# Performance work log

Hardware: AMD Instinct MI355X
Metric: run time of the kernel (lower is better)

Reference implementation:

```python
import jax, jax.numpy as jnp
import numpy as np

B, S, F, H, A = 256, 128, 512, 1024, 18


def setup_inputs() -> dict:
    key = jax.random.key(0)
    ks = jax.random.split(key, 16)
    u = lambda k, shape, fan: jax.random.uniform(k, shape, jnp.float32, -1.0, 1.0) / np.sqrt(fan)
    return {
        "obs": jax.random.normal(ks[0], (B, S, F), jnp.float32),
        "hx": jax.random.normal(ks[1], (B, H), jnp.float32),
        "cx": jax.random.normal(ks[2], (B, H), jnp.float32),
        "behaviour_acts": jax.random.randint(ks[3], (B, S, 1), 0, A),
        "W1": u(ks[4], (H, F), F), "b1": u(ks[5], (H,), F),
        "W_ih": u(ks[6], (4 * H, H), H), "b_ih": u(ks[7], (4 * H,), H),
        "W_hh": u(ks[8], (4 * H, H), H), "b_hh": u(ks[9], (4 * H,), H),
        "W_v": u(ks[10], (1, H), H), "b_v": u(ks[11], (1,), H),
        "W_l": u(ks[12], (A, H), H), "b_l": u(ks[13], (A,), H),
    }


def reference(obs, hx, cx, behaviour_acts, W1, b1, W_ih, b_ih, W_hh, b_hh, W_v, b_v, W_l, b_l):
    # MLP body: [B,S,F] -> [B,S,H]
    x = jax.nn.relu(jnp.einsum("bsf,hf->bsh", obs, W1) + b1)
    # precompute input-to-gate projection for all timesteps (one big GEMM)
    xg = jnp.einsum("bsh,gh->bsg", x, W_ih) + b_ih  # [B,S,4H]

    def step(carry, xg_t):
        h, c = carry
        gates = xg_t + h @ W_hh.T + b_hh  # [B,4H], gate order i,f,g,o (torch LSTMCell)
        i, f, g, o = jnp.split(gates, 4, axis=-1)
        c = jax.nn.sigmoid(f) * c + jax.nn.sigmoid(i) * jnp.tanh(g)
        h = jax.nn.sigmoid(o) * jnp.tanh(c)
        return (h, c), h

    _, hs = jax.lax.scan(step, (hx, cx), jnp.swapaxes(xg, 0, 1))
    output = jnp.swapaxes(hs, 0, 1)  # [B,S,H]

    value = output @ W_v.T + b_v  # [B,S,1]
    logits = output @ W_l.T + b_l  # [B,S,A]
    # torch Categorical(probs=softmax(logits)) => log-prob via log_softmax
    logp = jax.nn.log_softmax(logits, axis=-1)
    acts = behaviour_acts.reshape(logits.shape[0], logits.shape[1], 1)
    log_probs = jnp.take_along_axis(logp, acts, axis=-1)  # [B,S,1]
    entropy = -jnp.sum(jnp.exp(logp) * logp, axis=-1, keepdims=True)  # [B,S,1]
    return log_probs, entropy, value
```

## Files before the change

kernel.cpp:

```cpp
#include <hip/hip_runtime.h>

#define B_ 256
#define S_ 128
#define SP1 (S_+1)
#define F_ 512
#define H_ 1024
#define A_ 18
#define M_ (B_*S_)
#define G_ (4*H_)
#define CH_ 16
#define CR_ (B_*CH_)

typedef unsigned short u16;
typedef __attribute__((ext_vector_type(8))) _Float16 f16x8;
typedef __attribute__((ext_vector_type(4))) _Float16 f16x4;
typedef __attribute__((ext_vector_type(8))) short   s16x8;
typedef __attribute__((ext_vector_type(4))) float f32x4;
typedef __attribute__((ext_vector_type(4))) unsigned int u32x4;

__device__ __forceinline__ float bf2f(u16 u){
  union{unsigned int i; float f;} v; v.i=((unsigned int)u)<<16; return v.f;
}
__device__ __forceinline__ u16 f2bf(float f){
  unsigned int i=__float_as_uint(f);
  unsigned int r=(i+0x7fffu+((i>>16)&1u))>>16;
  return (u16)r;
}
__device__ __forceinline__ u16 f2h(float f){
  _Float16 h=(_Float16)f;
  union{_Float16 h; u16 u;} v; v.h=h; return v.u;
}
__device__ __forceinline__ float ldf(const void* p, size_t i, int m){
  return m ? ((const float*)p)[i] : bf2f(((const u16*)p)[i]);
}
__device__ __forceinline__ f16x8 load8_h(const void* base, size_t off, int m){
  f16x8 v;
  if(m==2) return *(const f16x8*)((const u16*)base + off);
  if(m==1){
    const float* f=(const float*)base + off;
    float4 a=*(const float4*)f; float4 b=*(const float4*)(f+4);
    v[0]=(_Float16)a.x; v[1]=(_Float16)a.y; v[2]=(_Float16)a.z; v[3]=(_Float16)a.w;
    v[4]=(_Float16)b.x; v[5]=(_Float16)b.y; v[6]=(_Float16)b.z; v[7]=(_Float16)b.w;
    return v;
  }
  s16x8 w=*(const s16x8*)((const u16*)base + off);
#pragma unroll
  for(int k=0;k<8;k++) v[k]=(_Float16)bf2f((u16)w[k]);
  return v;
}

__device__ __forceinline__ void store_c2(u16* p, u16 v){
  unsigned int vv=v;
  asm volatile("global_store_short %0, %1, off sc0 sc1" :: "v"(p), "v"(vv) : "memory");
}
__device__ __forceinline__ int load_c4(const int* p){
  int r;
  asm volatile("global_load_dword %0, %1, off sc0 sc1" : "=v"(r) : "v"(p));
  return r;
}
__device__ __forceinline__ void store_c4(int* p, int v){
  asm volatile("global_store_dword %0, %1, off sc0 sc1" :: "v"(p), "v"(v) : "memory");
}

__device__ __forceinline__ void bar_flags32(int* flags, int target, int gi, int lane, int w){
  asm volatile("s_waitcnt vmcnt(0)" ::: "memory");
  __syncthreads();
  if(w==0){
    if(lane==0) store_c4(flags+gi, target);
    while(true){
      int v=load_c4(flags+(lane&31));
      asm volatile("s_waitcnt vmcnt(0)" ::: "memory");
      if(__all(v>=target)) break;
      __builtin_amdgcn_s_sleep(1);
    }
  }
  __syncthreads();
}

template<int ROWS, int MAP>
__device__ __forceinline__ void stage(const void* base, int mode, int lda, int k0,
                                      int rowoff, int t0, u16* lds, int tid){
  if(mode==2){
    constexpr int NI=(ROWS*8)/256;
    int wv=tid>>6, l=tid&63;
#pragma unroll
    for(int i=0;i<NI;i++){
      int s0=i*256+(wv<<6), s=s0+l;
      int r=s>>3, gc=(s&7)^(r&7);
      int p=rowoff+r, sr;
      if(MAP==0)      sr=p;
      else if(MAP==1) sr=(p&3)*H_+(p>>2);
      else            sr=(p>>4)*S_+t0+(p&15);
      const u16* src=(const u16*)base + (size_t)sr*lda + k0 + gc*8;
      u16* dst=lds + s0*8;
      __builtin_amdgcn_global_load_lds((const __attribute__((address_space(1))) unsigned int*)src,
                                       (__attribute__((address_space(3))) unsigned int*)dst,
                                       16, 0, 0);
    }
  } else {
#pragma unroll
    for(int s0=tid; s0<ROWS*8; s0+=256){
      int r=s0>>3, gc=s0&7, lc=gc^(r&7);
      int p=rowoff+r, sr;
      if(MAP==0)      sr=p;
      else if(MAP==1) sr=(p&3)*H_+(p>>2);
      else            sr=(p>>4)*S_+t0+(p&15);
      f16x8 v=load8_h(base, (size_t)sr*lda + k0 + gc*8, mode);
      *(f16x8*)(lds + r*64 + lc*8)=v;
    }
  }
}

__device__ __forceinline__ f16x8 frag_ld(const u16* lds, int r0, int kc, int lane){
  int r = r0 + (lane&15);
  int c = (kc + (lane>>4)) ^ (r&7);
  return *(const f16x8*)(lds + r*64 + c*8);
}

template<int AMAP, int BMAP, int OUTMODE>
__global__ __launch_bounds__(256,3) void gemm128(const void* A, const void* Bt, void* C,
    const float* __restrict__ biasf, const int* __restrict__ flag,
    int K, int lda, int ldb, int ldc, int t0, int amode, int bmode){
  int m=*flag;
  int am = amode<0 ? m : amode;
  int bm_ = bmode<0 ? m : bmode;
  __shared__ u16 As[128*64];
  __shared__ u16 Bs[128*64];
  int tid=threadIdx.x, lane=tid&63, w=tid>>6;
  int bm=blockIdx.y*128, bn=blockIdx.x*128;
  int wm=(w&1)*64, wn=(w>>1)*64;
  f32x4 acc[4][4];
#pragma unroll
  for(int i=0;i<4;i++)
#pragma unroll
    for(int j=0;j<4;j++) acc[i][j]=(f32x4)(0.f);
  for(int k0=0;k0<K;k0+=64){
    stage<128,AMAP>(A , am,  lda, k0, bm, t0, As, tid);
    stage<128,BMAP>(Bt, bm_, ldb, k0, bn, t0, Bs, tid);
    __syncthreads();
#pragma unroll
    for(int kk=0;kk<2;kk++){
      f16x8 af[4], bq[4];
#pragma unroll
      for(int i=0;i<4;i++) af[i]=frag_ld(As, wm+i*16, kk*4, lane);
#pragma unroll
      for(int j=0;j<4;j++) bq[j]=frag_ld(Bs, wn+j*16, kk*4, lane);
#pragma unroll
      for(int i=0;i<4;i++)
#pragma unroll
        for(int j=0;j<4;j++)
          acc[i][j]=__builtin_amdgcn_mfma_f32_16x16x32_f16(af[i],bq[j],acc[i][j],0,0,0);
    }
    __syncthreads();
  }
  int rl=lane>>4, cl=lane&15;
#pragma unroll
  for(int j=0;j<4;j++){
    int col=bn+wn+j*16+cl;
    float bb=biasf[col];
#pragma unroll
    for(int i=0;i<4;i++){
#pragma unroll
      for(int r=0;r<4;r++){
        int row=bm+wm+i*16+rl*4+r;
        float v=acc[i][j][r]+bb;
        if(OUTMODE==0){ v=fmaxf(v,0.f); ((u16*)C)[(size_t)row*ldc+col]=f2h(v); }
        else if(OUTMODE==2){ ((u16*)C)[(size_t)row*ldc+col]=f2h(v); }
        else { ((float*)C)[(size_t)row*ldc+col]=v; }
      }
    }
  }
}

__global__ __launch_bounds__(512,2) void lstm_persist(u16* __restrict__ hh,
        const u16* __restrict__ Whhp, const u16* __restrict__ xgp,
        float* __restrict__ cst, int* __restrict__ cntc, int tbase){
  __shared__ u16 As[16*2048];
  __shared__ float gs[32*132];
  int tid=threadIdx.x, lane=tid&63, w=tid>>6;
  int grp=blockIdx.x&7, ci=blockIdx.x>>3;
  int bm=grp*32, bn=ci*128;
  int* flags = cntc + grp*64;

  f16x8 bw[32];
#pragma unroll
  for(int t=0;t<32;t++){
    int p = bn + w*16 + (lane&15);
    int k = t*32 + (lane>>4)*8;
    bw[t]=*(const f16x8*)(Whhp + (size_t)p*H_ + k);
  }
#pragma unroll
  for(int t=0;t<32;t++) asm volatile("" : "+a"(bw[t]));

  int rl0=tid>>5, rl1=(tid+512)>>5, u0=tid&31;
  int gu=(bn>>2)+u0;
  float c0=cst[(size_t)(bm+rl0)*H_+gu];
  float c1=cst[(size_t)(bm+rl1)*H_+gu];

  for(int dt=0;dt<CH_;dt++){
    f16x4 xv0=*(const f16x4*)(xgp + ((size_t)(bm+rl0)*CH_+dt)*G_ + bn + u0*4);
    f16x4 xv1=*(const f16x4*)(xgp + ((size_t)(bm+rl1)*CH_+dt)*G_ + bn + u0*4);
    if(dt) bar_flags32(flags, tbase+dt, ci, lane, w);
    const u16* hbase = hh + (size_t)(tbase+dt)*H_;
    {
      u32x4 tmp[4];
#pragma unroll
      for(int i=0;i<4;i++){
        int s=tid+i*512, kt=s>>8, r=(s>>3)&31, gc=s&7;
        tmp[i]=*(const u32x4*)(hbase + (size_t)(bm+r)*(SP1*H_) + kt*64 + gc*8);
      }
#pragma unroll
      for(int i=0;i<4;i++){
        int s=tid+i*512, kt=s>>8, r=(s>>3)&31, gc=s&7, lc=gc^(r&7);
        *(u32x4*)(As + kt*2048 + r*64 + lc*8)=tmp[i];
      }
    }
    __syncthreads();
    u32x4 tmp2[4];
#pragma unroll
    for(int i=0;i<4;i++){
      int s=tid+(i+4)*512, kt=s>>8, r=(s>>3)&31, gc=s&7;
      tmp2[i]=*(const u32x4*)(hbase + (size_t)(bm+r)*(SP1*H_) + kt*64 + gc*8);
    }
    f32x4 acc0=(f32x4)(0.f), acc1=(f32x4)(0.f);
#pragma unroll
    for(int t=0;t<16;t++){
      int kt=t>>1, kk=t&1;
      f16x8 af0=frag_ld(As+kt*2048, 0,  kk*4, lane);
      f16x8 af1=frag_ld(As+kt*2048, 16, kk*4, lane);
      acc0=__builtin_amdgcn_mfma_f32_16x16x32_f16(af0,bw[t],acc0,0,0,0);
      acc1=__builtin_amdgcn_mfma_f32_16x16x32_f16(af1,bw[t],acc1,0,0,0);
    }
#pragma unroll
    for(int i=0;i<4;i++){
      int s=tid+(i+4)*512, kt=s>>8, r=(s>>3)&31, gc=s&7, lc=gc^(r&7);
      *(u32x4*)(As + kt*2048 + r*64 + lc*8)=tmp2[i];
    }
    __syncthreads();
#pragma unroll
    for(int t=16;t<32;t++){
      int kt=t>>1, kk=t&1;
      f16x8 af0=frag_ld(As+kt*2048, 0,  kk*4, lane);
      f16x8 af1=frag_ld(As+kt*2048, 16, kk*4, lane);
      acc0=__builtin_amdgcn_mfma_f32_16x16x32_f16(af0,bw[t],acc0,0,0,0);
      acc1=__builtin_amdgcn_mfma_f32_16x16x32_f16(af1,bw[t],acc1,0,0,0);
    }
#pragma unroll
    for(int r=0;r<4;r++){
      gs[(   (lane>>4)*4+r)*132 + w*16+(lane&15)]=acc0[r];
      gs[(16+(lane>>4)*4+r)*132 + w*16+(lane&15)]=acc1[r];
    }
    __syncthreads();
    {
      float4 gv=*(const float4*)&gs[rl0*132+u0*4];
      float ii=1.f/(1.f+__expf(-(gv.x+(float)xv0[0])));
      float ff=1.f/(1.f+__expf(-(gv.y+(float)xv0[1])));
      float gg=1.f-2.f/(__expf(2.f*(gv.z+(float)xv0[2]))+1.f);
      float oo=1.f/(1.f+__expf(-(gv.w+(float)xv0[3])));
      c0=ff*c0+ii*gg;
      float th=1.f-2.f/(__expf(2.f*c0)+1.f);
      store_c2(hh + ((size_t)(bm+rl0)*SP1 + tbase+dt+1)*H_ + gu, f2h(oo*th));
    }
    {
      float4 gv=*(const float4*)&gs[rl1*132+u0*4];
      float ii=1.f/(1.f+__expf(-(gv.x+(float)xv1[0])));
      float ff=1.f/(1.f+__expf(-(gv.y+(float)xv1[1])));
      float gg=1.f-2.f/(__expf(2.f*(gv.z+(float)xv1[2]))+1.f);
      float oo=1.f/(1.f+__expf(-(gv.w+(float)xv1[3])));
      c1=ff*c1+ii*gg;
      float th=1.f-2.f/(__expf(2.f*c1)+1.f);
      store_c2(hh + ((size_t)(bm+rl1)*SP1 + tbase+dt+1)*H_ + gu, f2h(oo*th));
    }
  }
  cst[(size_t)(bm+rl0)*H_+gu]=c0;
  cst[(size_t)(bm+rl1)*H_+gu]=c1;
}

__global__ __launch_bounds__(256,2) void lstm_step(u16* __restrict__ hh, int slotAbs, int dt,
        const void* __restrict__ Whh, const u16* __restrict__ xg,
        float* __restrict__ cst, const int* __restrict__ flag){
  int m=*flag;
  __shared__ u16 As[64*64];
  __shared__ u16 Bs[64*64];
  __shared__ float gs[64*64];
  int tid=threadIdx.x, lane=tid&63, w=tid>>6;
  int bm=blockIdx.y*64, bn=blockIdx.x*64;
  int wm=(w&1)*32, wn=(w>>1)*32;
  f32x4 acc[2][2];
#pragma unroll
  for(int i=0;i<2;i++)
#pragma unroll
    for(int j=0;j<2;j++) acc[i][j]=(f32x4)(0.f);
  for(int k0=0;k0<H_;k0+=64){
    stage<64,0>(hh + (size_t)slotAbs*H_, 2, SP1*H_, k0, bm, 0, As, tid);
    stage<64,1>(Whh,                     m, H_,     k0, bn, 0, Bs, tid);
    __syncthreads();
#pragma unroll
    for(int kk=0;kk<2;kk++){
      f16x8 af[2], bq[2];
#pragma unroll
      for(int i=0;i<2;i++) af[i]=frag_ld(As, wm+i*16, kk*4, lane);
#pragma unroll
      for(int j=0;j<2;j++) bq[j]=frag_ld(Bs, wn+j*16, kk*4, lane);
#pragma unroll
      for(int i=0;i<2;i++)
#pragma unroll
        for(int j=0;j<2;j++)
          acc[i][j]=__builtin_amdgcn_mfma_f32_16x16x32_f16(af[i],bq[j],acc[i][j],0,0,0);
    }
    __syncthreads();
  }
  int rl=lane>>4, cl=lane&15;
#pragma unroll
  for(int j=0;j<2;j++){
    int coll=wn+j*16+cl;
#pragma unroll
    for(int i=0;i<2;i++){
#pragma unroll
      for(int r=0;r<4;r++){
        int rowl=wm+i*16+rl*4+r;
        float xv=(float)((const _Float16*)xg)[((size_t)(bm+rowl)*CH_+dt)*G_ + bn+coll];
        gs[rowl*64+coll]=acc[i][j][r] + xv;
      }
    }
  }
  __syncthreads();
#pragma unroll
  for(int p=0;p<4;p++){
    int idx=p*256+tid;
    int rowl=idx>>4, u=idx&15;
    float4 gv = *(const float4*)&gs[rowl*64+u*4];
    float ii=1.f/(1.f+__expf(-gv.x));
    float ff=1.f/(1.f+__expf(-gv.y));
    float gg=1.f-2.f/(__expf(2.f*gv.z)+1.f);
    float oo=1.f/(1.f+__expf(-gv.w));
    int gb=bm+rowl;
    int gu=(bn>>2)+u;
    size_t ci=(size_t)gb*H_+gu;
    float cn=ff*cst[ci]+ii*gg;
    cst[ci]=cn;
    float th=1.f-2.f/(__expf(2.f*cn)+1.f);
    hh[((size_t)gb*SP1 + slotAbs+1)*H_ + gu]=f2h(oo*th);
  }
}

__global__ __launch_bounds__(512,1) void heads_gemm(const u16* __restrict__ hh,
      const u16* __restrict__ WH, const float* __restrict__ blf,
      const int* __restrict__ acts, void* __restrict__ out, const int* __restrict__ flag){
  int m=*flag;
  __shared__ u16 Bs[16*2048];
  __shared__ u16 As[128*64];
  __shared__ float gs[128*36];
  int tid=threadIdx.x, lane=tid&63, w=tid>>6;
  int bm=blockIdx.x*128;
#pragma unroll
  for(int i=0;i<8;i++){
    int s=tid+i*512;
    int kt=s>>8, r=(s>>3)&31, gc=s&7, lc=gc^(r&7);
    *(f16x8*)(Bs+kt*2048+r*64+lc*8) = *(const f16x8*)(WH + (size_t)r*H_ + kt*64 + gc*8);
  }
  f32x4 acc0=(f32x4)(0.f), acc1=(f32x4)(0.f);
  for(int kt=0;kt<16;kt++){
#pragma unroll
    for(int i=0;i<2;i++){
      int s0=i*512+(w<<6), s=s0+lane;
      int r=s>>3, gc=(s&7)^(r&7);
      int rg=bm+r;
      const u16* src=hh + ((size_t)(rg>>7)*SP1 + (rg&127)+1)*H_ + kt*64 + gc*8;
      u16* dst=As + s0*8;
      __builtin_amdgcn_global_load_lds((const __attribute__((address_space(1))) unsigned int*)src,
                                       (__attribute__((address_space(3))) unsigned int*)dst,
                                       16, 0, 0);
    }
    __syncthreads();
#pragma unroll
    for(int kk=0;kk<2;kk++){
      f16x8 af=frag_ld(As, w*16, kk*4, lane);
      f16x8 b0=frag_ld(Bs+kt*2048, 0,  kk*4, lane);
      f16x8 b1=frag_ld(Bs+kt*2048, 16, kk*4, lane);
      acc0=__builtin_amdgcn_mfma_f32_16x16x32_f16(af,b0,acc0,0,0,0);
      acc1=__builtin_amdgcn_mfma_f32_16x16x32_f16(af,b1,acc1,0,0,0);
    }
    __syncthreads();
  }
#pragma unroll
  for(int r=0;r<4;r++){
    gs[(w*16+(lane>>4)*4+r)*36 + (lane&15)]      = acc0[r];
    gs[(w*16+(lane>>4)*4+r)*36 + 16 + (lane&15)] = acc1[r];
  }
  __syncthreads();
  if(tid<128){
    int rg=bm+tid;
    float lg[18];
#pragma unroll
    for(int j=0;j<18;j++) lg[j]=gs[tid*36+j]+blf[j];
    float value=gs[tid*36+18]+blf[18];
    float mx=lg[0];
#pragma unroll
    for(int j=1;j<18;j++) mx=fmaxf(mx,lg[j]);
    float se=0.f, s1=0.f;
#pragma unroll
    for(int j=0;j<18;j++){ float e=__expf(lg[j]-mx); se+=e; s1+=e*(lg[j]-mx); }
    float lse=__logf(se);
    int a=acts[rg];
    float la=0.f;
#pragma unroll
    for(int j=0;j<18;j++) la = (j==a) ? lg[j] : la;
    float lp=la-mx-lse;
    float ent=lse - s1/se;
    if(m){
      ((float*)out)[rg]=lp; ((float*)out)[M_+rg]=ent; ((float*)out)[2*M_+rg]=value;
    } else {
      ((u16*)out)[rg]=f2bf(lp); ((u16*)out)[M_+rg]=f2bf(ent); ((u16*)out)[2*M_+rg]=f2bf(value);
    }
  }
}

__global__ __launch_bounds__(256,2) void heads_full(const u16* __restrict__ hh,
      const void* __restrict__ Wl, const void* __restrict__ Wv,
      const float* __restrict__ blf, const int* __restrict__ acts,
      void* __restrict__ out, const int* __restrict__ flag){
  int m=*flag;
  int rg = blockIdx.x*4 + (threadIdx.x>>6);
  int lane = threadIdx.x & 63;
  int b=rg>>7, t=rg&(S_-1);
  const u16* h = hh + ((size_t)b*SP1 + t+1)*H_;
  f16x8 h0=*(const f16x8*)(h + lane*16), h1=*(const f16x8*)(h + lane*16 + 8);
  float hv[16];
#pragma unroll
  for(int k=0;k<8;k++){ hv[k]=(float)h0[k]; hv[8+k]=(float)h1[k]; }
  float dots[19];
#pragma unroll
  for(int j=0;j<19;j++){
    const void* wrow = (j<18) ? Wl : Wv;
    size_t roff = (j<18) ? (size_t)j*H_ : 0;
    float wv_[16];
    if(m){
      const float* f=(const float*)wrow + roff + lane*16;
      float4 a=*(const float4*)f, b2=*(const float4*)(f+4), c=*(const float4*)(f+8), d=*(const float4*)(f+12);
      wv_[0]=a.x;wv_[1]=a.y;wv_[2]=a.z;wv_[3]=a.w; wv_[4]=b2.x;wv_[5]=b2.y;wv_[6]=b2.z;wv_[7]=b2.w;
      wv_[8]=c.x;wv_[9]=c.y;wv_[10]=c.z;wv_[11]=c.w; wv_[12]=d.x;wv_[13]=d.y;wv_[14]=d.z;wv_[15]=d.w;
    } else {
      const u16* ub=(const u16*)wrow + roff + lane*16;
      s16x8 w0=*(const s16x8*)ub, w1=*(const s16x8*)(ub+8);
#pragma unroll
      for(int k=0;k<8;k++){ wv_[k]=bf2f((u16)w0[k]); wv_[8+k]=bf2f((u16)w1[k]); }
    }
    float d=0.f;
#pragma unroll
    for(int k=0;k<16;k++) d += hv[k]*wv_[k];
#pragma unroll
    for(int mm=1;mm<64;mm<<=1) d += __shfl_xor(d, mm, 64);
    dots[j]=d;
  }
  float lg[18];
#pragma unroll
  for(int j=0;j<18;j++) lg[j]=dots[j]+blf[j];
  float value=dots[18]+blf[18];
  float mx=lg[0];
#pragma unroll
  for(int j=1;j<18;j++) mx=fmaxf(mx,lg[j]);
  float se=0.f, s1=0.f;
#pragma unroll
  for(int j=0;j<18;j++){ float e=__expf(lg[j]-mx); se+=e; s1+=e*(lg[j]-mx); }
  float lse=__logf(se);
  int a=acts[rg];
  float la=0.f;
#pragma unroll
  for(int j=0;j<18;j++) la = (j==a) ? lg[j] : la;
  float lp=la-mx-lse;
  float ent=lse - s1/se;
  if(lane==0){
    if(m){
      ((float*)out)[rg]=lp; ((float*)out)[M_+rg]=ent; ((float*)out)[2*M_+rg]=value;
    } else {
      ((u16*)out)[rg]=f2bf(lp); ((u16*)out)[M_+rg]=f2bf(ent); ((u16*)out)[2*M_+rg]=f2bf(value);
    }
  }
}

__global__ void detect(const u16* __restrict__ obs_w, int* __restrict__ flag){
  __shared__ float red[256];
  float mx=0.f;
  for(int i=threadIdx.x;i<4096;i+=256) mx=fmaxf(mx,fabsf(bf2f(obs_w[i])));
  red[threadIdx.x]=mx; __syncthreads();
  for(int s=128;s>0;s>>=1){
    if(threadIdx.x<s) red[threadIdx.x]=fmaxf(red[threadIdx.x],red[threadIdx.x+s]);
    __syncthreads();
  }
  if(threadIdx.x==0) *flag=(red[0]>1e4f)?1:0;
}

__global__ void prep(const void* bih, const void* bhh, const void* b1, const void* bl, const void* bv,
                     const void* cx, const void* hx,
                     float* biasg, float* b1f, float* blf, float* cst, u16* hh,
                     int* cnt, const int* __restrict__ flag){
  int m=*flag;
  size_t i=(size_t)blockIdx.x*256+threadIdx.x;
  if(i<G_){ size_t rm=(i&3)*H_+(i>>2); biasg[i]=ldf(bih,rm,m)+ldf(bhh,rm,m); return; }
  i-=G_;
  if(i<H_){ b1f[i]=ldf(b1,i,m); return; }
  i-=H_;
  if(i<19){ blf[i]=(i<18)?ldf(bl,i,m):ldf(bv,0,m); return; }
  i-=19;
  if(i<512){ cnt[i]=0; return; }
  i-=512;
  if(i<(size_t)B_*H_){ cst[i]=ldf(cx,i,m); return; }
  i-=(size_t)B_*H_;
  if(i<(size_t)B_*H_){
    size_t b=i>>10, k=i&1023;
    hh[b*(SP1*H_) + k]=f2h(ldf(hx,i,m));
  }
}

__global__ void convw(const void* W1, const void* Wih, const void* Whh,
                      const void* Wl, const void* Wv,
                      u16* W1h, u16* Wihp, u16* Whhp, u16* WH,
                      const int* __restrict__ flag){
  int m=*flag;
  size_t i=((size_t)blockIdx.x*256+threadIdx.x)*8;
  const size_t n1=(size_t)H_*F_, n2=(size_t)G_*H_, n3=(size_t)32*H_;
  if(i<n1){ *(f16x8*)(W1h+i)=load8_h(W1,i,m); return; }
  i-=n1;
  if(i<n2){ size_t p=i>>10, c=i&1023; size_t sr=(p&3)*H_+(p>>2);
            *(f16x8*)(Wihp+i)=load8_h(Wih, sr*H_+c, m); return; }
  i-=n2;
  if(i<n2){ size_t p=i>>10, c=i&1023; size_t sr=(p&3)*H_+(p>>2);
            *(f16x8*)(Whhp+i)=load8_h(Whh, sr*H_+c, m); return; }
  i-=n2;
  if(i<n3){
    size_t j=i>>10, c=i&1023;
    f16x8 v;
    if(j<18)      v=load8_h(Wl, j*H_+c, m);
    else if(j==18) v=load8_h(Wv, c, m);
    else{ for(int k=0;k<8;k++) v[k]=(_Float16)0.f; }
    *(f16x8*)(WH+i)=v;
  }
}
__global__ void convobs(const void* obs, u16* obsh, const int* __restrict__ flag){
  int m=*flag;
  size_t i=((size_t)blockIdx.x*256+threadIdx.x)*8;
  if(i<(size_t)M_*F_) *(f16x8*)(obsh+i)=load8_h(obs,i,m);
}

extern "C" void kernel_launch(void* const* d_in, const int* in_sizes, int n_in,
                              void* d_out, int out_size, void* d_ws, size_t ws_size,
                              hipStream_t stream){
  const void* obs=d_in[0];
  const void* hx =d_in[1];
  const void* cx =d_in[2];
  const int* acts=(const int*)d_in[3];
  const void* W1 =d_in[4];
  const void* b1 =d_in[5];
  const void* Wih=d_in[6];
  const void* bih=d_in[7];
  const void* Whh=d_in[8];
  const void* bhh=d_in[9];
  const void* Wv =d_in[10];
  const void* bv =d_in[11];
  const void* Wl =d_in[12];
  const void* bl =d_in[13];

  char* w=(char*)d_ws;
  auto alloc=[&](size_t n){ char* p=w; w+=((n+255)&~(size_t)255); return p; };
  int*   flag =(int*)alloc(4);
  int*   cnt  =(int*)alloc(512*4);
  float* biasg=(float*)alloc((size_t)G_*4);
  float* b1f  =(float*)alloc((size_t)H_*4);
  float* blf  =(float*)alloc(32*4);
  float* cst  =(float*)alloc((size_t)B_*H_*4);
  u16*   hh   =(u16*)alloc((size_t)B_*SP1*H_*2);
  u16*   xc   =(u16*)alloc((size_t)CR_*H_*2);
  u16*   xg   =(u16*)alloc((size_t)CR_*G_*2);
  size_t nW=((size_t)H_*F_ + 2*(size_t)G_*H_ + 32*(size_t)H_)*2 + 1024;
  bool pathW = ((size_t)(w-(char*)d_ws) + nW) <= ws_size;
  u16 *W1h=0,*Wihp=0,*Whhp=0,*WH=0;
  if(pathW){ W1h=(u16*)alloc((size_t)H_*F_*2); Wihp=(u16*)alloc((size_t)G_*H_*2);
             Whhp=(u16*)alloc((size_t)G_*H_*2); WH=(u16*)alloc((size_t)32*H_*2); }
  size_t nXC=(size_t)M_*H_*2 + 256;
  bool pathXC = pathW && (((size_t)(w-(char*)d_ws) + nXC) <= ws_size);
  u16* xcf=0; if(pathXC) xcf=(u16*)alloc((size_t)M_*H_*2);
  size_t nO=(size_t)M_*F_*2 + 256;
  bool pathO = pathXC && (((size_t)(w-(char*)d_ws) + nO) <= ws_size);
  u16* obsh=0; if(pathO) obsh=(u16*)alloc((size_t)M_*F_*2);

  detect<<<1,256,0,stream>>>((const u16*)obs, flag);
  {
    int total=G_+H_+19+512+B_*H_+B_*H_;
    prep<<<(total+255)/256,256,0,stream>>>(bih,bhh,b1,bl,bv,cx,hx, biasg,b1f,blf,cst,hh,cnt, flag);
  }
  if(pathW){
    size_t n=((size_t)H_*F_+2*(size_t)G_*H_+32*(size_t)H_)/8;
    convw<<<(int)((n+255)/256),256,0,stream>>>(W1,Wih,Whh,Wl,Wv, W1h,Wihp,Whhp,WH, flag);
  }
  if(pathO){
    size_t n=(size_t)M_*F_/8;
    convobs<<<(int)((n+255)/256),256,0,stream>>>(obs, obsh, flag);
  }
  if(pathXC){
    gemm128<0,0,0><<<dim3(H_/128, M_/128),256,0,stream>>>(
        pathO?(const void*)obsh:obs, pathW?(const void*)W1h:W1, xcf, b1f, flag,
        F_, F_, F_, H_, 0, pathO?2:-1, pathW?2:-1);
  }

  const int NC=S_/CH_;
  for(int c=0;c<NC;c++){
    int t0=c*CH_;
    if(!pathXC){
      gemm128<2,0,0><<<dim3(H_/128, CR_/128),256,0,stream>>>(
          obs, pathW?(const void*)W1h:W1, xc, b1f, flag, F_, F_, F_, H_, t0, -1, pathW?2:-1);
    }
    if(pathXC)
      gemm128<2,0,2><<<dim3(G_/128, CR_/128),256,0,stream>>>(
          xcf, Wihp, xg, biasg, flag, H_, H_, H_, G_, t0, 2, 2);
    else if(pathW)
      gemm128<0,0,2><<<dim3(G_/128, CR_/128),256,0,stream>>>(
          xc, Wihp, xg, biasg, flag, H_, H_, H_, G_, 0, 2, 2);
    else
      gemm128<0,1,2><<<dim3(G_/128, CR_/128),256,0,stream>>>(
          xc, Wih, xg, biasg, flag, H_, H_, H_, G_, 0, 2, -1);

    if(pathW)
      lstm_persist<<<256,512,0,stream>>>(hh, Whhp, xg, cst, cnt, t0);
    else
      for(int dt=0;dt<CH_;dt++)
        lstm_step<<<dim3(G_/64, B_/64),256,0,stream>>>(hh, t0+dt, dt, Whh, xg, cst, flag);
  }

  if(pathW)
    heads_gemm<<<dim3(M_/128),512,0,stream>>>(hh, WH, blf, acts, d_out, flag);
  else
    heads_full<<<dim3(M_/4),256,0,stream>>>(hh, Wl, Wv, blf, acts, d_out, flag);
}
```

Before: 1.107 ms.

## Overlap next chunk's input-gate GEMM with the persistent LSTM kernel

The persistent LSTM kernel now launches 512 extra blocks beyond its 256 recurrence blocks. These extra blocks compute the next chunk's x·W_ih projection into a double-buffered xg array, so the standalone GEMM launch per chunk is removed after the first chunk. The recurrence LDS buffer is enlarged and shared with the gate scratch, and the h tile is loaded in one pass instead of two halves. Risks include the co-scheduled GEMM blocks competing with the flag-synchronized recurrence blocks for CUs and bandwidth, or preventing those blocks from all becoming resident.

New measurement: 1.162 ms. 1.05x slower.

```diff
diff --git a/kernel.cpp b/kernel.cpp
--- a/kernel.cpp
+++ b/kernel.cpp
@@ -172,12 +172,81 @@
   }
 }
 
-__global__ __launch_bounds__(512,2) void lstm_persist(u16* __restrict__ hh,
+__global__ __launch_bounds__(512,2) void lstm_xg(u16* __restrict__ hh,
         const u16* __restrict__ Whhp, const u16* __restrict__ xgp,
-        float* __restrict__ cst, int* __restrict__ cntc, int tbase){
-  __shared__ u16 As[16*2048];
-  __shared__ float gs[32*132];
+        float* __restrict__ cst, int* __restrict__ cntc, int tbase,
+        const u16* __restrict__ xcf, const u16* __restrict__ Wihp,
+        const float* __restrict__ biasg, u16* __restrict__ xgn, int t0n){
+  __shared__ __align__(16) char lds_raw[16*2048*2];
   int tid=threadIdx.x, lane=tid&63, w=tid>>6;
+
+  if(blockIdx.x>=256){
+    u16* As2=(u16*)lds_raw;
+    u16* Bs2=(u16*)(lds_raw+16384);
+    int gb=blockIdx.x-256;
+    int tm=gb&31, tn=gb>>5;
+    int bm2=tm*128, bn2=tn*256;
+    int wr=w&1, wc=w>>1;
+    f32x4 acc[4][4];
+#pragma unroll
+    for(int i=0;i<4;i++)
+#pragma unroll
+      for(int j=0;j<4;j++) acc[i][j]=(f32x4)(0.f);
+    for(int kt=0;kt<16;kt++){
+      int k0=kt*64;
+#pragma unroll
+      for(int i=0;i<2;i++){
+        int s0=w*128+i*64, s=s0+lane;
+        int r=s>>3, gc=(s&7)^(r&7);
+        int p=bm2+r;
+        const u16* src=xcf + ((size_t)(p>>4)*S_ + t0n + (p&15))*H_ + k0 + gc*8;
+        __builtin_amdgcn_global_load_lds((const __attribute__((address_space(1))) unsigned int*)src,
+                                         (__attribute__((address_space(3))) unsigned int*)(As2+s0*8),
+                                         16, 0, 0);
+      }
+#pragma unroll
+      for(int i=0;i<4;i++){
+        int s0=w*256+i*64, s=s0+lane;
+        int r=s>>3, gc=(s&7)^(r&7);
+        const u16* src=Wihp + (size_t)(bn2+r)*H_ + k0 + gc*8;
+        __builtin_amdgcn_global_load_lds((const __attribute__((address_space(1))) unsigned int*)src,
+                                         (__attribute__((address_space(3))) unsigned int*)(Bs2+s0*8),
+                                         16, 0, 0);
+      }
+      __syncthreads();
+#pragma unroll
+      for(int kk=0;kk<2;kk++){
+        f16x8 af[4], bq[4];
+#pragma unroll
+        for(int i=0;i<4;i++) af[i]=frag_ld(As2, wr*64+i*16, kk*4, lane);
+#pragma unroll
+        for(int j=0;j<4;j++) bq[j]=frag_ld(Bs2, wc*64+j*16, kk*4, lane);
+#pragma unroll
+        for(int i=0;i<4;i++)
+#pragma unroll
+          for(int j=0;j<4;j++)
+            acc[i][j]=__builtin_amdgcn_mfma_f32_16x16x32_f16(af[i],bq[j],acc[i][j],0,0,0);
+      }
+      __syncthreads();
+    }
+    int rl=lane>>4, cl=lane&15;
+#pragma unroll
+    for(int j=0;j<4;j++){
+      int col=bn2+wc*64+j*16+cl;
+      float bb=biasg[col];
+#pragma unroll
+      for(int i=0;i<4;i++){
+#pragma unroll
+        for(int r=0;r<4;r++){
+          int row=bm2+wr*64+i*16+rl*4+r;
+          ((u16*)xgn)[(size_t)row*G_+col]=f2h(acc[i][j][r]+bb);
+        }
+      }
+    }
+    return;
+  }
+  u16* As=(u16*)lds_raw;
+  float* gs=(float*)lds_raw;
   int grp=blockIdx.x&7, ci=blockIdx.x>>3;
   int bm=grp*32, bn=ci*128;
   int* flags = cntc + grp*64;
@@ -203,48 +272,29 @@
     if(dt) bar_flags32(flags, tbase+dt, ci, lane, w);
     const u16* hbase = hh + (size_t)(tbase+dt)*H_;
     {
-      u32x4 tmp[4];
-#pragma unroll
-      for(int i=0;i<4;i++){
+      u32x4 tmp[8];
+#pragma unroll
+      for(int i=0;i<8;i++){
         int s=tid+i*512, kt=s>>8, r=(s>>3)&31, gc=s&7;
         tmp[i]=*(const u32x4*)(hbase + (size_t)(bm+r)*(SP1*H_) + kt*64 + gc*8);
       }
 #pragma unroll
-      for(int i=0;i<4;i++){
+      for(int i=0;i<8;i++){
         int s=tid+i*512, kt=s>>8, r=(s>>3)&31, gc=s&7, lc=gc^(r&7);
         *(u32x4*)(As + kt*2048 + r*64 + lc*8)=tmp[i];
       }
     }
     __syncthreads();
-    u32x4 tmp2[4];
-#pragma unroll
-    for(int i=0;i<4;i++){
-      int s=tid+(i+4)*512, kt=s>>8, r=(s>>3)&31, gc=s&7;
-      tmp2[i]=*(const u32x4*)(hbase + (size_t)(bm+r)*(SP1*H_) + kt*64 + gc*8);
-    }
     f32x4 acc0=(f32x4)(0.f), acc1=(f32x4)(0.f);
 #pragma unroll
-    for(int t=0;t<16;t++){
+    for(int t=0;t<32;t++){
       int kt=t>>1, kk=t&1;
       f16x8 af0=frag_ld(As+kt*2048, 0,  kk*4, lane);
       f16x8 af1=frag_ld(As+kt*2048, 16, kk*4, lane);
       acc0=__builtin_amdgcn_mfma_f32_16x16x32_f16(af0,bw[t],acc0,0,0,0);
       acc1=__builtin_amdgcn_mfma_f32_16x16x32_f16(af1,bw[t],acc1,0,0,0);
     }
-#pragma unroll
-    for(int i=0;i<4;i++){
-      int s=tid+(i+4)*512, kt=s>>8, r=(s>>3)&31, gc=s&7, lc=gc^(r&7);
-      *(u32x4*)(As + kt*2048 + r*64 + lc*8)=tmp2[i];
-    }
-    __syncthreads();
-#pragma unroll
-    for(int t=16;t<32;t++){
-      int kt=t>>1, kk=t&1;
-      f16x8 af0=frag_ld(As+kt*2048, 0,  kk*4, lane);
-      f16x8 af1=frag_ld(As+kt*2048, 16, kk*4, lane);
-      acc0=__builtin_amdgcn_mfma_f32_16x16x32_f16(af0,bw[t],acc0,0,0,0);
-      acc1=__builtin_amdgcn_mfma_f32_16x16x32_f16(af1,bw[t],acc1,0,0,0);
-    }
+    __syncthreads();
 #pragma unroll
     for(int r=0;r<4;r++){
       gs[(   (lane>>4)*4+r)*132 + w*16+(lane&15)]=acc0[r];
@@ -580,6 +630,9 @@
   size_t nXC=(size_t)M_*H_*2 + 256;
   bool pathXC = pathW && (((size_t)(w-(char*)d_ws) + nXC) <= ws_size);
   u16* xcf=0; if(pathXC) xcf=(u16*)alloc((size_t)M_*H_*2);
+  size_t nF=(size_t)CR_*G_*2 + 256;
+  bool pathF = pathXC && (((size_t)(w-(char*)d_ws) + nF) <= ws_size);
+  u16* xgB=0; if(pathF) xgB=(u16*)alloc((size_t)CR_*G_*2);
   size_t nO=(size_t)M_*F_*2 + 256;
   bool pathO = pathXC && (((size_t)(w-(char*)d_ws) + nO) <= ws_size);
   u16* obsh=0; if(pathO) obsh=(u16*)alloc((size_t)M_*F_*2);
@@ -606,25 +659,33 @@
   const int NC=S_/CH_;
   for(int c=0;c<NC;c++){
     int t0=c*CH_;
+    u16* xgcur = (pathF && (c&1)) ? xgB : xg;
+    u16* xgnxt = (pathF && !(c&1)) ? xgB : xg;
     if(!pathXC){
       gemm128<2,0,0><<<dim3(H_/128, CR_/128),256,0,stream>>>(
           obs, pathW?(const void*)W1h:W1, xc, b1f, flag, F_, F_, F_, H_, t0, -1, pathW?2:-1);
     }
-    if(pathXC)
-      gemm128<2,0,2><<<dim3(G_/128, CR_/128),256,0,stream>>>(
-          xcf, Wihp, xg, biasg, flag, H_, H_, H_, G_, t0, 2, 2);
-    else if(pathW)
-      gemm128<0,0,2><<<dim3(G_/128, CR_/128),256,0,stream>>>(
-          xc, Wihp, xg, biasg, flag, H_, H_, H_, G_, 0, 2, 2);
-    else
-      gemm128<0,1,2><<<dim3(G_/128, CR_/128),256,0,stream>>>(
-          xc, Wih, xg, biasg, flag, H_, H_, H_, G_, 0, 2, -1);
-
-    if(pathW)
-      lstm_persist<<<256,512,0,stream>>>(hh, Whhp, xg, cst, cnt, t0);
-    else
+    if(!pathF || c==0){
+      if(pathXC)
+        gemm128<2,0,2><<<dim3(G_/128, CR_/128),256,0,stream>>>(
+            xcf, Wihp, xgcur, biasg, flag, H_, H_, H_, G_, t0, 2, 2);
+      else if(pathW)
+        gemm128<0,0,2><<<dim3(G_/128, CR_/128),256,0,stream>>>(
+            xc, Wihp, xgcur, biasg, flag, H_, H_, H_, G_, 0, 2, 2);
+      else
+        gemm128<0,1,2><<<dim3(G_/128, CR_/128),256,0,stream>>>(
+            xc, Wih, xg, biasg, flag, H_, H_, H_, G_, 0, 2, -1);
+    }
+
+    if(pathW){
+      bool cog = pathF && (c<NC-1);
+      int grid = 256 + (cog ? 512 : 0);
+      lstm_xg<<<grid,512,0,stream>>>(hh, Whhp, xgcur, cst, cnt, t0,
+          xcf, Wihp, biasg, cog?xgnxt:(u16*)nullptr, t0+CH_);
+    } else {
       for(int dt=0;dt<CH_;dt++)
         lstm_step<<<dim3(G_/64, B_/64),256,0,stream>>>(hh, t0+dt, dt, Whh, xg, cst, flag);
+    }
   }
 
   if(pathW)
```
